# Kernel optimization log

Measured on AMD Instinct MI355X. Metric: run time of the kernel, lower is better.

Reference implementation:

```python
import jax, jax.numpy as jnp
import numpy as np

B, D, PRE, NEXT, SC, ANT = 1000, 8, 98, 512, 32, 5  # batch, devices, split-in, split-out, subcarriers, antennas
TAU = 0.1  # noise std (tau2 in original torch.normal(0, tau2, ...))


def setup_inputs() -> dict:
    key = jax.random.key(0)
    ks = jax.random.split(key, 18)
    rn = lambda k, s, sc=0.05: (jax.random.normal(k, s, jnp.float32) * sc)
    return {
        "x": jax.random.normal(ks[0], (B, D * PRE), jnp.float32),
        "noise": jax.random.normal(ks[1], (B, SC, ANT), jnp.float32) * TAU,
        "sub_w": rn(ks[2], (D, PRE, NEXT)),
        "sub_b": rn(ks[3], (D, NEXT)),
        "ln_gamma": jnp.ones((D, NEXT), jnp.float32),
        "ln_beta": jnp.zeros((D, NEXT), jnp.float32),
        "cut_w": rn(ks[4], (D, NEXT, SC)),
        "cut_b": rn(ks[5], (D, SC)),
        "b_mat": rn(ks[6], (D, SC), 1.0),
        "h_mat": rn(ks[7], (D, SC, ANT), 1.0),
        "a_mat": rn(ks[8], (SC, ANT), 1.0),
        "cut_layer_bias": rn(ks[9], (SC,)),
        "fc3_w": rn(ks[10], (SC, 98)),
        "fc3_b": rn(ks[11], (98,)),
        "fc4_w": rn(ks[12], (98, 49)),
        "fc4_b": rn(ks[13], (49,)),
        "out_w": rn(ks[14], (49, 10)),
        "out_b": rn(ks[15], (10,)),
        "k_idx": jax.random.permutation(ks[16], SC).astype(jnp.int32),  # one-hot indicator_mat as index map
    }


def reference(x, noise, sub_w, sub_b, ln_gamma, ln_beta, cut_w, cut_b,
              b_mat, h_mat, a_mat, cut_layer_bias,
              fc3_w, fc3_b, fc4_w, fc4_b, out_w, out_b, k_idx):
    # split x into per-device chunks: torch.split along dim=1 with uniform sizes
    xs = x.reshape(B, D, PRE).transpose(1, 0, 2)                       # (D, B, PRE)
    h = jax.nn.relu(jnp.einsum('dbi,dio->dbo', xs, sub_w) + sub_b[:, None, :])
    mu = jnp.mean(h, axis=-1, keepdims=True)
    var = jnp.mean(jnp.square(h - mu), axis=-1, keepdims=True)
    h = (h - mu) * jax.lax.rsqrt(var + 1e-5) * ln_gamma[:, None, :] + ln_beta[:, None, :]
    cut = jax.nn.relu(jnp.einsum('dbo,doc->dbc', h, cut_w) + cut_b[:, None, :])  # (D, B, SC)
    # h_vec[n, j] = a_j^T h_mat[n, k(j)]  (indicator one-hot -> gather)
    h_sel = h_mat[:, k_idx, :]                                         # (D, SC, ANT)
    h_vec = jnp.einsum('dkc,kc->dk', h_sel, a_mat)                     # (D, SC)
    # received = sum_n (cut_n * b_n) * h_vec_n
    received = jnp.einsum('dbc,dc,dc->bc', cut, b_mat, h_vec)          # (B, SC)
    scaled_noise = jnp.einsum('bjc,jc->bj', noise, a_mat)              # (B, SC)
    z = jax.nn.relu(received + scaled_noise + cut_layer_bias)
    z = jax.nn.relu(z @ fc3_w + fc3_b)
    z = jax.nn.relu(z @ fc4_w + fc4_b)
    return jax.nn.log_softmax(z @ out_w + out_b, axis=1)
```

## Files before the change

### kernel.cpp

```cpp
#include <hip/hip_runtime.h>
#include <math.h>

#define B 1000
#define D 8
#define PRE 98
#define NEXT 512
#define SC 32
#define ANT 5
#define BM 32
#define NTILE 32
#define KP 128

using bf16x8 = __attribute__((ext_vector_type(8))) short;
using f32x4  = __attribute__((ext_vector_type(4))) float;

static __device__ __forceinline__ unsigned short f2bf(float f) {
    union { float f; unsigned u; } v{f};
    unsigned r = (v.u + 0x7fffu + ((v.u >> 16) & 1u)) >> 16;
    return (unsigned short)r;
}
static __device__ __forceinline__ float bf2f(unsigned short h) {
    union { unsigned u; float f; } v{(unsigned)h << 16};
    return v.f;
}

__global__ __launch_bounds__(256) void k_prep(const float* __restrict__ sub_w,
                                              const float* __restrict__ cut_w,
                                              unsigned short* __restrict__ sub_wT,
                                              unsigned short* __restrict__ cut_wT) {
    __shared__ __align__(16) unsigned short tile[32][128];
    int t = threadIdx.x, bid = blockIdx.x;
    if (bid < 128) {
        int d = bid >> 4, n0 = (bid & 15) * 32;
        int nn = t & 31, kk = t >> 5;
#pragma unroll
        for (int j = 0; j < 16; ++j) {
            int k = j * 8 + kk;
            float v = (k < PRE) ? sub_w[(d * PRE + k) * NEXT + n0 + nn] : 0.f;
            tile[nn][k] = f2bf(v);
        }
        __syncthreads();
        int row = t >> 3, c0 = (t & 7) * 16;
        unsigned short* dst = sub_wT + ((size_t)(d * NEXT + n0 + row)) * KP + c0;
        *reinterpret_cast<bf16x8*>(dst)     = *reinterpret_cast<bf16x8*>(&tile[row][c0]);
        *reinterpret_cast<bf16x8*>(dst + 8) = *reinterpret_cast<bf16x8*>(&tile[row][c0 + 8]);
    } else {
        int bb = bid - 128;
        int d = bb >> 2, k0 = (bb & 3) * 128;
        int nn = t & 31, kk = t >> 5;
#pragma unroll
        for (int j = 0; j < 16; ++j) {
            int kl = j * 8 + kk;
            tile[nn][kl] = f2bf(cut_w[(d * NEXT + k0 + kl) * SC + nn]);
        }
        __syncthreads();
        int row = t >> 3, c0 = (t & 7) * 16;
        unsigned short* dst = cut_wT + ((size_t)(d * SC + row)) * NEXT + k0 + c0;
        *reinterpret_cast<bf16x8*>(dst)     = *reinterpret_cast<bf16x8*>(&tile[row][c0]);
        *reinterpret_cast<bf16x8*>(dst + 8) = *reinterpret_cast<bf16x8*>(&tile[row][c0 + 8]);
    }
}

__global__ __launch_bounds__(512, 2) void k_mid(const float* __restrict__ x,
                                                const unsigned short* __restrict__ sub_wT,
                                                const float* __restrict__ sub_b,
                                                const float* __restrict__ gamma,
                                                const float* __restrict__ beta,
                                                const unsigned short* __restrict__ cut_wT,
                                                const float* __restrict__ cut_b,
                                                const float* __restrict__ b_mat,
                                                const float* __restrict__ h_mat,
                                                const float* __restrict__ a_mat,
                                                const int* __restrict__ k_idx,
                                                float* __restrict__ part) {
    __shared__ __align__(16) unsigned short x_lds[BM][136];
    __shared__ __align__(16) unsigned short h_lds[BM][536];
    __shared__ f32x4 pacc[4][64];

    int t = threadIdx.x;
    int d = blockIdx.x >> 5;
    int tile = blockIdx.x & 31;
    int b0 = tile * BM;

    for (int idx = t; idx < BM * 136; idx += 512) {
        int r = idx / 136, i = idx - r * 136;
        int b = b0 + r;
        float v = (b < B && i < PRE) ? x[b * (D * PRE) + d * PRE + i] : 0.f;
        x_lds[r][i] = f2bf(v);
    }
    __syncthreads();

    int w = t >> 6, lane = t & 63;
    int lr = lane >> 4, lc = lane & 15;

    {
        int n0 = w * 64;
        const unsigned short* bw = sub_wT + (size_t)d * NEXT * KP + (size_t)(n0 + lc) * KP + lr * 8;
        bf16x8 bq[4][4];
#pragma unroll
        for (int ks = 0; ks < 4; ++ks)
#pragma unroll
            for (int nf = 0; nf < 4; ++nf)
                bq[ks][nf] = *reinterpret_cast<const bf16x8*>(bw + (size_t)nf * 16 * KP + ks * 32);

        f32x4 acc[2][4] = {};
#pragma unroll
        for (int ks = 0; ks < 4; ++ks) {
            bf16x8 a0 = *reinterpret_cast<const bf16x8*>(&x_lds[lc][ks * 32 + lr * 8]);
            bf16x8 a1 = *reinterpret_cast<const bf16x8*>(&x_lds[16 + lc][ks * 32 + lr * 8]);
#pragma unroll
            for (int nf = 0; nf < 4; ++nf) {
                acc[0][nf] = __builtin_amdgcn_mfma_f32_16x16x32_bf16(a0, bq[ks][nf], acc[0][nf], 0, 0, 0);
                acc[1][nf] = __builtin_amdgcn_mfma_f32_16x16x32_bf16(a1, bq[ks][nf], acc[1][nf], 0, 0, 0);
            }
        }
        const float* sb = sub_b + d * NEXT;
#pragma unroll
        for (int nf = 0; nf < 4; ++nf) {
            int n = n0 + nf * 16 + lc;
            float bias = sb[n];
#pragma unroll
            for (int mt = 0; mt < 2; ++mt)
#pragma unroll
                for (int r = 0; r < 4; ++r)
                    h_lds[mt * 16 + lr * 4 + r][n] = f2bf(fmaxf(acc[mt][nf][r] + bias, 0.f));
        }
    }
    __syncthreads();

    {
        int row = t >> 4, l16 = t & 15;
        unsigned int* hrow = reinterpret_cast<unsigned int*>(&h_lds[row][0]);
        float s1 = 0.f, s2 = 0.f;
#pragma unroll
        for (int j = 0; j < 16; ++j) {
            unsigned int p = hrow[l16 + j * 16];
            float v0 = bf2f((unsigned short)(p & 0xffffu));
            float v1 = bf2f((unsigned short)(p >> 16));
            s1 += v0 + v1;
            s2 += v0 * v0 + v1 * v1;
        }
#pragma unroll
        for (int off = 8; off >= 1; off >>= 1) {
            s1 += __shfl_xor(s1, off, 16);
            s2 += __shfl_xor(s2, off, 16);
        }
        float mu = s1 * (1.f / NEXT);
        float var = s2 * (1.f / NEXT) - mu * mu;
        float rs = rsqrtf(var + 1e-5f);
        const float* g = gamma + d * NEXT;
        const float* be = beta + d * NEXT;
#pragma unroll
        for (int j = 0; j < 16; ++j) {
            int pi = l16 + j * 16;
            unsigned int p = hrow[pi];
            int n = pi * 2;
            float v0 = (bf2f((unsigned short)(p & 0xffffu)) - mu) * rs * g[n] + be[n];
            float v1 = (bf2f((unsigned short)(p >> 16)) - mu) * rs * g[n + 1] + be[n + 1];
            hrow[pi] = (unsigned)f2bf(v0) | ((unsigned)f2bf(v1) << 16);
        }
    }
    __syncthreads();

    {
        int kh = w >> 2, sub = w & 3;
        int mt = sub >> 1, nt = sub & 1;
        int kbase = kh * 256;
        const unsigned short* bw = cut_wT + (size_t)(d * SC + nt * 16 + lc) * NEXT + kbase + lr * 8;
        bf16x8 bq[8];
#pragma unroll
        for (int ks = 0; ks < 8; ++ks)
            bq[ks] = *reinterpret_cast<const bf16x8*>(bw + ks * 32);

        f32x4 acc = {};
#pragma unroll
        for (int ks = 0; ks < 8; ++ks) {
            bf16x8 a = *reinterpret_cast<const bf16x8*>(&h_lds[mt * 16 + lc][kbase + ks * 32 + lr * 8]);
            acc = __builtin_amdgcn_mfma_f32_16x16x32_bf16(a, bq[ks], acc, 0, 0, 0);
        }
        if (kh == 1) pacc[sub][lane] = acc;
        __syncthreads();
        if (kh == 0) {
            f32x4 o = pacc[sub][lane];
            acc[0] += o[0]; acc[1] += o[1]; acc[2] += o[2]; acc[3] += o[3];
            int c = nt * 16 + lc;
            int kk = k_idx[c];
            float hv = 0.f;
#pragma unroll
            for (int a = 0; a < ANT; ++a)
                hv = fmaf(h_mat[(d * SC + kk) * ANT + a], a_mat[c * ANT + a], hv);
            float cf = b_mat[d * SC + c] * hv;
            float cb = cut_b[d * SC + c];
#pragma unroll
            for (int r = 0; r < 4; ++r) {
                int m = mt * 16 + lr * 4 + r;
                int b = b0 + m;
                if (b < B) part[(b * D + d) * SC + c] = fmaxf(acc[r] + cb, 0.f) * cf;
            }
        }
    }
}

__global__ __launch_bounds__(512) void k_tail(const float* __restrict__ part,
                                              const float* __restrict__ noise,
                                              const float* __restrict__ a_mat,
                                              const float* __restrict__ clb,
                                              const float* __restrict__ fc3_w,
                                              const float* __restrict__ fc3_b,
                                              const float* __restrict__ fc4_w,
                                              const float* __restrict__ fc4_b,
                                              const float* __restrict__ out_w,
                                              const float* __restrict__ out_b,
                                              float* __restrict__ out) {
    __shared__ float w3[SC * 98];
    __shared__ float w4[98 * 49];
    __shared__ float wo[49 * 10];
    __shared__ float b3[98], b4[49], bo[10], clb_s[SC], am_s[SC * ANT];
    __shared__ float z_s[8][SC];
    __shared__ float z3_s[8][98];
    __shared__ float z4_s[8][49];

    int t = threadIdx.x;
    for (int i = t; i < SC * 98; i += 512) w3[i] = fc3_w[i];
    for (int i = t; i < 98 * 49; i += 512) w4[i] = fc4_w[i];
    for (int i = t; i < 49 * 10; i += 512) wo[i] = out_w[i];
    if (t < 98) b3[t] = fc3_b[t];
    if (t < 49) b4[t] = fc4_b[t];
    if (t < 10) bo[t] = out_b[t];
    if (t >= 128 && t < 128 + SC) clb_s[t - 128] = clb[t - 128];
    if (t >= 192 && t < 192 + SC * ANT) am_s[t - 192] = a_mat[t - 192];
    __syncthreads();

    int w = t >> 6, lane = t & 63;
    int b = blockIdx.x * 8 + w;

    {
        float4 v = *reinterpret_cast<const float4*>(part + (size_t)b * (D * SC) + lane * 4);
#pragma unroll
        for (int off = 8; off <= 32; off <<= 1) {
            v.x += __shfl_xor(v.x, off);
            v.y += __shfl_xor(v.y, off);
            v.z += __shfl_xor(v.z, off);
            v.w += __shfl_xor(v.w, off);
        }
        if (lane < 8) {
            int cc = lane * 4;
            float s[4] = {v.x, v.y, v.z, v.w};
#pragma unroll
            for (int i = 0; i < 4; ++i) {
                int c = cc + i;
                float zz = s[i] + clb_s[c];
#pragma unroll
                for (int a = 0; a < ANT; ++a)
                    zz = fmaf(noise[(b * SC + c) * ANT + a], am_s[c * ANT + a], zz);
                z_s[w][c] = fmaxf(zz, 0.f);
            }
        }
    }

    for (int o = lane; o < 98; o += 64) {
        float s = b3[o];
#pragma unroll
        for (int j = 0; j < SC; ++j) s = fmaf(z_s[w][j], w3[j * 98 + o], s);
        z3_s[w][o] = fmaxf(s, 0.f);
    }
    if (lane < 49) {
        float s = b4[lane];
        for (int j = 0; j < 98; ++j) s = fmaf(z3_s[w][j], w4[j * 49 + lane], s);
        z4_s[w][lane] = fmaxf(s, 0.f);
    }
    float v = -INFINITY;
    if (lane < 10) {
        float s = bo[lane];
        for (int j = 0; j < 49; ++j) s = fmaf(z4_s[w][j], wo[j * 10 + lane], s);
        v = s;
    }
    float mx = v;
#pragma unroll
    for (int off = 8; off >= 1; off >>= 1) mx = fmaxf(mx, __shfl_xor(mx, off, 16));
    float e = (lane < 10) ? expf(v - mx) : 0.f;
    float ssum = e;
#pragma unroll
    for (int off = 8; off >= 1; off >>= 1) ssum += __shfl_xor(ssum, off, 16);
    if (lane < 10) out[b * 10 + lane] = v - mx - logf(ssum);
}

extern "C" void kernel_launch(void* const* d_in, const int* in_sizes, int n_in,
                              void* d_out, int out_size, void* d_ws, size_t ws_size,
                              hipStream_t stream) {
    const float* x      = (const float*)d_in[0];
    const float* noise  = (const float*)d_in[1];
    const float* sub_w  = (const float*)d_in[2];
    const float* sub_b  = (const float*)d_in[3];
    const float* ln_g   = (const float*)d_in[4];
    const float* ln_b   = (const float*)d_in[5];
    const float* cut_w  = (const float*)d_in[6];
    const float* cut_b  = (const float*)d_in[7];
    const float* b_mat  = (const float*)d_in[8];
    const float* h_mat  = (const float*)d_in[9];
    const float* a_mat  = (const float*)d_in[10];
    const float* clb    = (const float*)d_in[11];
    const float* fc3_w  = (const float*)d_in[12];
    const float* fc3_b  = (const float*)d_in[13];
    const float* fc4_w  = (const float*)d_in[14];
    const float* fc4_b  = (const float*)d_in[15];
    const float* out_w  = (const float*)d_in[16];
    const float* out_b  = (const float*)d_in[17];
    const int*   k_idx  = (const int*)d_in[18];
    float* out = (float*)d_out;

    char* ws = (char*)d_ws;
    float* part            = (float*)ws;
    unsigned short* sub_wT = (unsigned short*)(ws + (1 << 20));
    unsigned short* cut_wT = (unsigned short*)(ws + (2 << 20));

    k_prep<<<160, 256, 0, stream>>>(sub_w, cut_w, sub_wT, cut_wT);
    k_mid<<<D * NTILE, 512, 0, stream>>>(x, sub_wT, sub_b, ln_g, ln_b, cut_wT,
                                         cut_b, b_mat, h_mat, a_mat, k_idx, part);
    k_tail<<<125, 512, 0, stream>>>(part, noise, a_mat, clb, fc3_w, fc3_b,
                                    fc4_w, fc4_b, out_w, out_b, out);
}
```

Measured before the change: 30.24 us.

## Prefetch weights early in k_mid, drop split-K cut GEMM, hoist part load in tail

In k_mid the sub_w fragments are now loaded before the x tile is staged, and the cut_w fragments plus per-channel scale and bias are loaded before layer norm. This overlaps global-load latency with the LDS staging and normalization phases. The cut GEMM no longer splits K across two wave halves with an LDS partial-sum exchange and extra barrier; four waves each do the full K=512 while the other four sit idle. The launch-bounds occupancy hint is dropped, and k_tail issues its part load before filling the weight LDS. The extra live registers (16 more bf16x8 per thread) may lower occupancy.

```diff
diff --git a/kernel.cpp b/kernel.cpp
--- a/kernel.cpp
+++ b/kernel.cpp
@@ -61,26 +61,37 @@
     }
 }
 
-__global__ __launch_bounds__(512, 2) void k_mid(const float* __restrict__ x,
-                                                const unsigned short* __restrict__ sub_wT,
-                                                const float* __restrict__ sub_b,
-                                                const float* __restrict__ gamma,
-                                                const float* __restrict__ beta,
-                                                const unsigned short* __restrict__ cut_wT,
-                                                const float* __restrict__ cut_b,
-                                                const float* __restrict__ b_mat,
-                                                const float* __restrict__ h_mat,
-                                                const float* __restrict__ a_mat,
-                                                const int* __restrict__ k_idx,
-                                                float* __restrict__ part) {
+__global__ __launch_bounds__(512) void k_mid(const float* __restrict__ x,
+                                             const unsigned short* __restrict__ sub_wT,
+                                             const float* __restrict__ sub_b,
+                                             const float* __restrict__ gamma,
+                                             const float* __restrict__ beta,
+                                             const unsigned short* __restrict__ cut_wT,
+                                             const float* __restrict__ cut_b,
+                                             const float* __restrict__ b_mat,
+                                             const float* __restrict__ h_mat,
+                                             const float* __restrict__ a_mat,
+                                             const int* __restrict__ k_idx,
+                                             float* __restrict__ part) {
     __shared__ __align__(16) unsigned short x_lds[BM][136];
     __shared__ __align__(16) unsigned short h_lds[BM][536];
-    __shared__ f32x4 pacc[4][64];
 
     int t = threadIdx.x;
     int d = blockIdx.x >> 5;
     int tile = blockIdx.x & 31;
     int b0 = tile * BM;
+
+    int w = t >> 6, lane = t & 63;
+    int lr = lane >> 4, lc = lane & 15;
+
+    int n0 = w * 64;
+    const unsigned short* bw = sub_wT + (size_t)d * NEXT * KP + (size_t)(n0 + lc) * KP + lr * 8;
+    bf16x8 bq[4][4];
+#pragma unroll
+    for (int ks = 0; ks < 4; ++ks)
+#pragma unroll
+        for (int nf = 0; nf < 4; ++nf)
+            bq[ks][nf] = *reinterpret_cast<const bf16x8*>(bw + (size_t)nf * 16 * KP + ks * 32);
 
     for (int idx = t; idx < BM * 136; idx += 512) {
         int r = idx / 136, i = idx - r * 136;
@@ -90,30 +101,37 @@
     }
     __syncthreads();
 
-    int w = t >> 6, lane = t & 63;
-    int lr = lane >> 4, lc = lane & 15;
+    f32x4 acc[2][4] = {};
+#pragma unroll
+    for (int ks = 0; ks < 4; ++ks) {
+        bf16x8 a0 = *reinterpret_cast<const bf16x8*>(&x_lds[lc][ks * 32 + lr * 8]);
+        bf16x8 a1 = *reinterpret_cast<const bf16x8*>(&x_lds[16 + lc][ks * 32 + lr * 8]);
+#pragma unroll
+        for (int nf = 0; nf < 4; ++nf) {
+            acc[0][nf] = __builtin_amdgcn_mfma_f32_16x16x32_bf16(a0, bq[ks][nf], acc[0][nf], 0, 0, 0);
+            acc[1][nf] = __builtin_amdgcn_mfma_f32_16x16x32_bf16(a1, bq[ks][nf], acc[1][nf], 0, 0, 0);
+        }
+    }
+
+    bf16x8 gq[16];
+    float cf = 0.f, cb = 0.f;
+    if (w < 4) {
+        int nt = w & 1;
+        const unsigned short* cw = cut_wT + (size_t)(d * SC + nt * 16 + lc) * NEXT + lr * 8;
+#pragma unroll
+        for (int ks = 0; ks < 16; ++ks)
+            gq[ks] = *reinterpret_cast<const bf16x8*>(cw + ks * 32);
+        int c = nt * 16 + lc;
+        int kk = k_idx[c];
+        float hv = 0.f;
+#pragma unroll
+        for (int a = 0; a < ANT; ++a)
+            hv = fmaf(h_mat[(d * SC + kk) * ANT + a], a_mat[c * ANT + a], hv);
+        cf = b_mat[d * SC + c] * hv;
+        cb = cut_b[d * SC + c];
+    }
 
     {
-        int n0 = w * 64;
-        const unsigned short* bw = sub_wT + (size_t)d * NEXT * KP + (size_t)(n0 + lc) * KP + lr * 8;
-        bf16x8 bq[4][4];
-#pragma unroll
-        for (int ks = 0; ks < 4; ++ks)
-#pragma unroll
-            for (int nf = 0; nf < 4; ++nf)
-                bq[ks][nf] = *reinterpret_cast<const bf16x8*>(bw + (size_t)nf * 16 * KP + ks * 32);
-
-        f32x4 acc[2][4] = {};
-#pragma unroll
-        for (int ks = 0; ks < 4; ++ks) {
-            bf16x8 a0 = *reinterpret_cast<const bf16x8*>(&x_lds[lc][ks * 32 + lr * 8]);
-            bf16x8 a1 = *reinterpret_cast<const bf16x8*>(&x_lds[16 + lc][ks * 32 + lr * 8]);
-#pragma unroll
-            for (int nf = 0; nf < 4; ++nf) {
-                acc[0][nf] = __builtin_amdgcn_mfma_f32_16x16x32_bf16(a0, bq[ks][nf], acc[0][nf], 0, 0, 0);
-                acc[1][nf] = __builtin_amdgcn_mfma_f32_16x16x32_bf16(a1, bq[ks][nf], acc[1][nf], 0, 0, 0);
-            }
-        }
         const float* sb = sub_b + d * NEXT;
 #pragma unroll
         for (int nf = 0; nf < 4; ++nf) {
@@ -162,41 +180,20 @@
     }
     __syncthreads();
 
-    {
-        int kh = w >> 2, sub = w & 3;
-        int mt = sub >> 1, nt = sub & 1;
-        int kbase = kh * 256;
-        const unsigned short* bw = cut_wT + (size_t)(d * SC + nt * 16 + lc) * NEXT + kbase + lr * 8;
-        bf16x8 bq[8];
-#pragma unroll
-        for (int ks = 0; ks < 8; ++ks)
-            bq[ks] = *reinterpret_cast<const bf16x8*>(bw + ks * 32);
-
-        f32x4 acc = {};
-#pragma unroll
-        for (int ks = 0; ks < 8; ++ks) {
-            bf16x8 a = *reinterpret_cast<const bf16x8*>(&h_lds[mt * 16 + lc][kbase + ks * 32 + lr * 8]);
-            acc = __builtin_amdgcn_mfma_f32_16x16x32_bf16(a, bq[ks], acc, 0, 0, 0);
-        }
-        if (kh == 1) pacc[sub][lane] = acc;
-        __syncthreads();
-        if (kh == 0) {
-            f32x4 o = pacc[sub][lane];
-            acc[0] += o[0]; acc[1] += o[1]; acc[2] += o[2]; acc[3] += o[3];
-            int c = nt * 16 + lc;
-            int kk = k_idx[c];
-            float hv = 0.f;
-#pragma unroll
-            for (int a = 0; a < ANT; ++a)
-                hv = fmaf(h_mat[(d * SC + kk) * ANT + a], a_mat[c * ANT + a], hv);
-            float cf = b_mat[d * SC + c] * hv;
-            float cb = cut_b[d * SC + c];
-#pragma unroll
-            for (int r = 0; r < 4; ++r) {
-                int m = mt * 16 + lr * 4 + r;
-                int b = b0 + m;
-                if (b < B) part[(b * D + d) * SC + c] = fmaxf(acc[r] + cb, 0.f) * cf;
-            }
+    if (w < 4) {
+        int mt = w >> 1, nt = w & 1;
+        f32x4 acc2 = {};
+#pragma unroll
+        for (int ks = 0; ks < 16; ++ks) {
+            bf16x8 a = *reinterpret_cast<const bf16x8*>(&h_lds[mt * 16 + lc][ks * 32 + lr * 8]);
+            acc2 = __builtin_amdgcn_mfma_f32_16x16x32_bf16(a, gq[ks], acc2, 0, 0, 0);
+        }
+        int c = nt * 16 + lc;
+#pragma unroll
+        for (int r = 0; r < 4; ++r) {
+            int m = mt * 16 + lr * 4 + r;
+            int b = b0 + m;
+            if (b < B) part[(b * D + d) * SC + c] = fmaxf(acc2[r] + cb, 0.f) * cf;
         }
     }
 }
@@ -221,6 +218,11 @@
     __shared__ float z4_s[8][49];
 
     int t = threadIdx.x;
+    int w = t >> 6, lane = t & 63;
+    int b = blockIdx.x * 8 + w;
+
+    float4 v = *reinterpret_cast<const float4*>(part + (size_t)b * (D * SC) + lane * 4);
+
     for (int i = t; i < SC * 98; i += 512) w3[i] = fc3_w[i];
     for (int i = t; i < 98 * 49; i += 512) w4[i] = fc4_w[i];
     for (int i = t; i < 49 * 10; i += 512) wo[i] = out_w[i];
@@ -231,11 +233,7 @@
     if (t >= 192 && t < 192 + SC * ANT) am_s[t - 192] = a_mat[t - 192];
     __syncthreads();
 
-    int w = t >> 6, lane = t & 63;
-    int b = blockIdx.x * 8 + w;
-
     {
-        float4 v = *reinterpret_cast<const float4*>(part + (size_t)b * (D * SC) + lane * 4);
 #pragma unroll
         for (int off = 8; off <= 32; off <<= 1) {
             v.x += __shfl_xor(v.x, off);
@@ -269,20 +267,20 @@
         for (int j = 0; j < 98; ++j) s = fmaf(z3_s[w][j], w4[j * 49 + lane], s);
         z4_s[w][lane] = fmaxf(s, 0.f);
     }
-    float v = -INFINITY;
+    float vv = -INFINITY;
     if (lane < 10) {
         float s = bo[lane];
         for (int j = 0; j < 49; ++j) s = fmaf(z4_s[w][j], wo[j * 10 + lane], s);
-        v = s;
-    }
-    float mx = v;
+        vv = s;
+    }
+    float mx = vv;
 #pragma unroll
     for (int off = 8; off >= 1; off >>= 1) mx = fmaxf(mx, __shfl_xor(mx, off, 16));
-    float e = (lane < 10) ? expf(v - mx) : 0.f;
+    float e = (lane < 10) ? expf(vv - mx) : 0.f;
     float ssum = e;
 #pragma unroll
     for (int off = 8; off >= 1; off >>= 1) ssum += __shfl_xor(ssum, off, 16);
-    if (lane < 10) out[b * 10 + lane] = v - mx - logf(ssum);
+    if (lane < 10) out[b * 10 + lane] = vv - mx - logf(ssum);
 }
 
 extern "C" void kernel_launch(void* const* d_in, const int* in_sizes, int n_in,
```

Result: slower. 31.32 us (+3.6%).
